# Kernel optimization log

Measured on AMD Instinct MI355X. Metric: run time of the kernel, lower is better.

Reference implementation:

```python
import jax, jax.numpy as jnp
import numpy as np

BN_EPS = 1e-5
LEAKY_SLOPE = 0.01

N_TOTAL, FEAT_DIM = 100000, 128
N_BATCH, K = 50000, 16
EMBED_DIM = 128


def setup_inputs() -> dict:
    key = jax.random.key(0)
    k1, k2, k3 = jax.random.split(key, 3)
    raw_features = jax.random.normal(k1, (N_TOTAL, FEAT_DIM), dtype=jnp.float32)
    weight = jax.random.normal(k2, (FEAT_DIM, EMBED_DIM), dtype=jnp.float32) * (1.0 / np.sqrt(FEAT_DIM))
    gamma = jnp.ones((EMBED_DIM,), dtype=jnp.float32)
    beta = jnp.zeros((EMBED_DIM,), dtype=jnp.float32)
    neigh_idx = jax.random.randint(k3, (N_BATCH, K), 0, N_TOTAL, dtype=jnp.int64)
    return {"raw_features": raw_features, "weight": weight, "gamma": gamma,
            "beta": beta, "neigh_idx": neigh_idx}


def reference(raw_features, weight, gamma, beta, neigh_idx):
    # Mean aggregation over sampled neighbors: [N_BATCH, K, F] -> [N_BATCH, F]
    neigh_feats = jnp.mean(raw_features[neigh_idx], axis=1)
    # Dense transform: [N_BATCH, EMBED_DIM]
    x = neigh_feats @ weight
    # BatchNorm1d (training mode: batch statistics, biased variance)
    mean = jnp.mean(x, axis=0)
    var = jnp.var(x, axis=0)
    x = (x - mean) * jax.lax.rsqrt(var + BN_EPS) * gamma + beta
    # LeakyReLU (default negative_slope=0.01)
    return jnp.where(x >= 0, x, LEAKY_SLOPE * x)
```

## Files before the change

kernel.cpp:

```cpp
#include <hip/hip_runtime.h>
#include <hip/hip_bf16.h>


#define NTOTAL 100000
#define FEAT   128
#define NB     50000
#define KNEI   16
#define NTILES (NB / 16)

#define OFF_STATS 0
#define OFF_WT    1024
#define OFF_RAWB  33792
#define OFF_XB    (33792 + 25600000)
#define WS_NEEDED (OFF_XB + 12800000)

typedef float f32x4 __attribute__((ext_vector_type(4)));
typedef short bf16x8 __attribute__((ext_vector_type(8)));

__device__ __forceinline__ unsigned short f2bf(float f) {
    union { float f; unsigned u; } v; v.f = f;
    unsigned r = v.u + 0x7FFF + ((v.u >> 16) & 1);
    return (unsigned short)(r >> 16);
}

#define WT_LD 136
#define A_LD  136

__global__ __launch_bounds__(256) void enc_conv(
    const float* __restrict__ raw, const float* __restrict__ W,
    unsigned short* __restrict__ rawb, unsigned short* __restrict__ Wt,
    float* __restrict__ gstats)
{
    const int t = threadIdx.x;
    if (blockIdx.x < 64) {
        int e = blockIdx.x * 256 + t;
        int n = e >> 7, k = e & 127;
        Wt[e] = f2bf(W[k * FEAT + n]);
    }
    if (blockIdx.x == 64 && t < 2 * FEAT) gstats[t] = 0.f;

    const float4* raw4 = (const float4*)raw;
    ushort4* rb4 = (ushort4*)rawb;
    const int NQ = NTOTAL * FEAT / 4;
    for (int e = blockIdx.x * 256 + t; e < NQ; e += gridDim.x * 256) {
        float4 v = raw4[e];
        ushort4 b;
        b.x = f2bf(v.x); b.y = f2bf(v.y); b.z = f2bf(v.z); b.w = f2bf(v.w);
        rb4[e] = b;
    }
}

__global__ __launch_bounds__(256, 4) void enc_gemm_b(
    const unsigned short* __restrict__ rawb, const unsigned short* __restrict__ Wt,
    const int* __restrict__ idx, unsigned short* __restrict__ xb,
    float* __restrict__ gstats)
{
    __shared__ unsigned short sWt[128 * WT_LD];
    __shared__ unsigned short sA[16 * A_LD];
    __shared__ int sidx[256];

    const int t = threadIdx.x;

    #pragma unroll
    for (int i = 0; i < 8; ++i) {
        int e = t + i * 256;
        int n = e >> 4, c = e & 15;
        *(uint4*)&sWt[n * WT_LD + c * 8] = *(const uint4*)&Wt[n * 128 + c * 8];
    }

    const int lane = t & 63;
    const int wv = t >> 6;
    const int ln = lane & 15;
    const int qd = lane >> 4;
    const int c2 = t & 15;
    const int g  = t >> 4;
    const int n0 = wv * 32 + ln, n1 = n0 + 16;

    float s1a = 0.f, s2a = 0.f, s1b = 0.f, s2b = 0.f;

    for (int tile = blockIdx.x; tile < NTILES; tile += gridDim.x) {
        const int i0 = tile * 16;
        __syncthreads();
        sidx[t] = idx[i0 * KNEI + t];
        __syncthreads();

        {
            const int* ip = &sidx[g * KNEI];
            uint4 v[16];
            #pragma unroll
            for (int k = 0; k < KNEI; ++k)
                v[k] = *(const uint4*)&rawb[(size_t)ip[k] * FEAT + c2 * 8];
            __builtin_amdgcn_sched_barrier(0);
            float a0=0.f,a1=0.f,a2=0.f,a3=0.f,a4=0.f,a5=0.f,a6=0.f,a7=0.f;
            #pragma unroll
            for (int k = 0; k < KNEI; ++k) {
                a0 += __uint_as_float(v[k].x << 16);
                a1 += __uint_as_float(v[k].x & 0xFFFF0000u);
                a2 += __uint_as_float(v[k].y << 16);
                a3 += __uint_as_float(v[k].y & 0xFFFF0000u);
                a4 += __uint_as_float(v[k].z << 16);
                a5 += __uint_as_float(v[k].z & 0xFFFF0000u);
                a6 += __uint_as_float(v[k].w << 16);
                a7 += __uint_as_float(v[k].w & 0xFFFF0000u);
            }
            uint4 b;
            b.x = (unsigned)f2bf(a0 * 0.0625f) | ((unsigned)f2bf(a1 * 0.0625f) << 16);
            b.y = (unsigned)f2bf(a2 * 0.0625f) | ((unsigned)f2bf(a3 * 0.0625f) << 16);
            b.z = (unsigned)f2bf(a4 * 0.0625f) | ((unsigned)f2bf(a5 * 0.0625f) << 16);
            b.w = (unsigned)f2bf(a6 * 0.0625f) | ((unsigned)f2bf(a7 * 0.0625f) << 16);
            *(uint4*)&sA[g * A_LD + c2 * 8] = b;
        }
        __syncthreads();

        f32x4 acc0 = {0.f, 0.f, 0.f, 0.f}, acc1 = {0.f, 0.f, 0.f, 0.f};
        #pragma unroll
        for (int kt = 0; kt < 4; ++kt) {
            const int k0 = kt * 32 + qd * 8;
            bf16x8 a  = *(const bf16x8*)&sA[ln * A_LD + k0];
            bf16x8 b0 = *(const bf16x8*)&sWt[n0 * WT_LD + k0];
            bf16x8 b1 = *(const bf16x8*)&sWt[n1 * WT_LD + k0];
            acc0 = __builtin_amdgcn_mfma_f32_16x16x32_bf16(a, b0, acc0, 0, 0, 0);
            acc1 = __builtin_amdgcn_mfma_f32_16x16x32_bf16(a, b1, acc1, 0, 0, 0);
        }

        #pragma unroll
        for (int ri = 0; ri < 4; ++ri) {
            const int row = i0 + qd * 4 + ri;
            float v0 = acc0[ri], v1 = acc1[ri];
            xb[row * FEAT + n0] = f2bf(v0);
            xb[row * FEAT + n1] = f2bf(v1);
            s1a += v0; s2a += v0 * v0;
            s1b += v1; s2b += v1 * v1;
        }
    }

    s1a += __shfl_down(s1a, 32); s1a += __shfl_down(s1a, 16);
    s2a += __shfl_down(s2a, 32); s2a += __shfl_down(s2a, 16);
    s1b += __shfl_down(s1b, 32); s1b += __shfl_down(s1b, 16);
    s2b += __shfl_down(s2b, 32); s2b += __shfl_down(s2b, 16);
    if (qd == 0) {
        atomicAdd(&gstats[n0], s1a);
        atomicAdd(&gstats[FEAT + n0], s2a);
        atomicAdd(&gstats[n1], s1b);
        atomicAdd(&gstats[FEAT + n1], s2b);
    }
}

__global__ __launch_bounds__(256) void enc_bn_b(
    const unsigned short* __restrict__ xb, float* __restrict__ out,
    const float* __restrict__ gstats,
    const float* __restrict__ gamma, const float* __restrict__ beta)
{
    __shared__ float sScale[FEAT], sShift[FEAT];
    const int t = threadIdx.x;
    if (t < FEAT) {
        float s1 = gstats[t], s2 = gstats[FEAT + t];
        float mean = s1 * (1.0f / NB);
        float var = s2 * (1.0f / NB) - mean * mean;
        float sc = gamma[t] * rsqrtf(var + 1e-5f);
        sScale[t] = sc;
        sShift[t] = beta[t] - mean * sc;
    }
    __syncthreads();

    const int f8 = (t & 15) * 8;
    const float4 sc0 = *(const float4*)&sScale[f8], sc1 = *(const float4*)&sScale[f8 + 4];
    const float4 sh0 = *(const float4*)&sShift[f8], sh1 = *(const float4*)&sShift[f8 + 4];

    const uint4* x4 = (const uint4*)xb;
    float4* o4 = (float4*)out;
    const int total8 = NB * FEAT / 8;
    for (int e = blockIdx.x * 256 + t; e < total8; e += gridDim.x * 256) {
        uint4 v = x4[e];
        float4 r0, r1; float y;
        y = __uint_as_float(v.x << 16)        * sc0.x + sh0.x; r0.x = (y >= 0.f) ? y : 0.01f * y;
        y = __uint_as_float(v.x & 0xFFFF0000u)* sc0.y + sh0.y; r0.y = (y >= 0.f) ? y : 0.01f * y;
        y = __uint_as_float(v.y << 16)        * sc0.z + sh0.z; r0.z = (y >= 0.f) ? y : 0.01f * y;
        y = __uint_as_float(v.y & 0xFFFF0000u)* sc0.w + sh0.w; r0.w = (y >= 0.f) ? y : 0.01f * y;
        y = __uint_as_float(v.z << 16)        * sc1.x + sh1.x; r1.x = (y >= 0.f) ? y : 0.01f * y;
        y = __uint_as_float(v.z & 0xFFFF0000u)* sc1.y + sh1.y; r1.y = (y >= 0.f) ? y : 0.01f * y;
        y = __uint_as_float(v.w << 16)        * sc1.z + sh1.z; r1.z = (y >= 0.f) ? y : 0.01f * y;
        y = __uint_as_float(v.w & 0xFFFF0000u)* sc1.w + sh1.w; r1.w = (y >= 0.f) ? y : 0.01f * y;
        o4[e * 2] = r0; o4[e * 2 + 1] = r1;
    }
}

__global__ __launch_bounds__(256, 4) void enc_gemm_f(
    const float* __restrict__ raw, const float* __restrict__ W,
    const int* __restrict__ idx, float* __restrict__ out,
    float* __restrict__ gstats)
{
    __shared__ unsigned short sWt[128 * WT_LD];
    __shared__ unsigned short sA[16 * A_LD];
    __shared__ int sidx[256];
    const int t = threadIdx.x;
    #pragma unroll 4
    for (int i = 0; i < 64; ++i) {
        int e = t + i * 256;
        int f = e >> 7, n = e & 127;
        sWt[n * WT_LD + f] = f2bf(W[e]);
    }
    const int lane = t & 63, wv = t >> 6, ln = lane & 15, qd = lane >> 4;
    const int c = t & 31, g = t >> 5;
    const int n0 = wv * 32 + ln, n1 = n0 + 16;
    float s1a = 0.f, s2a = 0.f, s1b = 0.f, s2b = 0.f;
    const float4* raw4 = (const float4*)raw;
    for (int tile = blockIdx.x; tile < NTILES; tile += gridDim.x) {
        const int i0 = tile * 16;
        __syncthreads();
        sidx[t] = idx[i0 * KNEI + t];
        __syncthreads();
        #pragma unroll
        for (int rr = 0; rr < 2; ++rr) {
            const int r = g * 2 + rr;
            const int* ip = &sidx[r * KNEI];
            float4 acc = {0.f, 0.f, 0.f, 0.f};
            #pragma unroll
            for (int k = 0; k < KNEI; ++k) {
                float4 v = raw4[(size_t)ip[k] * 32 + c];
                acc.x += v.x; acc.y += v.y; acc.z += v.z; acc.w += v.w;
            }
            ushort4 b;
            b.x = f2bf(acc.x * 0.0625f); b.y = f2bf(acc.y * 0.0625f);
            b.z = f2bf(acc.z * 0.0625f); b.w = f2bf(acc.w * 0.0625f);
            *(ushort4*)&sA[r * A_LD + c * 4] = b;
        }
        __syncthreads();
        f32x4 acc0 = {0.f, 0.f, 0.f, 0.f}, acc1 = {0.f, 0.f, 0.f, 0.f};
        #pragma unroll
        for (int kt = 0; kt < 4; ++kt) {
            const int k0 = kt * 32 + qd * 8;
            bf16x8 a  = *(const bf16x8*)&sA[ln * A_LD + k0];
            bf16x8 b0 = *(const bf16x8*)&sWt[n0 * WT_LD + k0];
            bf16x8 b1 = *(const bf16x8*)&sWt[n1 * WT_LD + k0];
            acc0 = __builtin_amdgcn_mfma_f32_16x16x32_bf16(a, b0, acc0, 0, 0, 0);
            acc1 = __builtin_amdgcn_mfma_f32_16x16x32_bf16(a, b1, acc1, 0, 0, 0);
        }
        #pragma unroll
        for (int ri = 0; ri < 4; ++ri) {
            const int row = i0 + qd * 4 + ri;
            float v0 = acc0[ri], v1 = acc1[ri];
            out[row * FEAT + n0] = v0;
            out[row * FEAT + n1] = v1;
            s1a += v0; s2a += v0 * v0;
            s1b += v1; s2b += v1 * v1;
        }
    }
    s1a += __shfl_down(s1a, 32); s1a += __shfl_down(s1a, 16);
    s2a += __shfl_down(s2a, 32); s2a += __shfl_down(s2a, 16);
    s1b += __shfl_down(s1b, 32); s1b += __shfl_down(s1b, 16);
    s2b += __shfl_down(s2b, 32); s2b += __shfl_down(s2b, 16);
    if (qd == 0) {
        atomicAdd(&gstats[n0], s1a);
        atomicAdd(&gstats[FEAT + n0], s2a);
        atomicAdd(&gstats[n1], s1b);
        atomicAdd(&gstats[FEAT + n1], s2b);
    }
}

__global__ __launch_bounds__(256) void enc_bn_f(
    float* __restrict__ out, const float* __restrict__ gstats,
    const float* __restrict__ gamma, const float* __restrict__ beta)
{
    __shared__ float sScale[FEAT], sShift[FEAT];
    const int t = threadIdx.x;
    if (t < FEAT) {
        float s1 = gstats[t], s2 = gstats[FEAT + t];
        float mean = s1 * (1.0f / NB);
        float var = s2 * (1.0f / NB) - mean * mean;
        float sc = gamma[t] * rsqrtf(var + 1e-5f);
        sScale[t] = sc;
        sShift[t] = beta[t] - mean * sc;
    }
    __syncthreads();
    const int f4 = (t & 31) * 4;
    const float4 sc = *(const float4*)&sScale[f4];
    const float4 sh = *(const float4*)&sShift[f4];
    const int total4 = NB * FEAT / 4;
    float4* o4 = (float4*)out;
    for (int e = blockIdx.x * 256 + t; e < total4; e += gridDim.x * 256) {
        float4 v = o4[e];
        float4 r; float y;
        y = v.x * sc.x + sh.x; r.x = (y >= 0.f) ? y : 0.01f * y;
        y = v.y * sc.y + sh.y; r.y = (y >= 0.f) ? y : 0.01f * y;
        y = v.z * sc.z + sh.z; r.z = (y >= 0.f) ? y : 0.01f * y;
        y = v.w * sc.w + sh.w; r.w = (y >= 0.f) ? y : 0.01f * y;
        o4[e] = r;
    }
}

extern "C" void kernel_launch(void* const* d_in, const int* in_sizes, int n_in,
                              void* d_out, int out_size, void* d_ws, size_t ws_size,
                              hipStream_t stream) {
    const float* raw   = (const float*)d_in[0];
    const float* W     = (const float*)d_in[1];
    const float* gamma = (const float*)d_in[2];
    const float* beta  = (const float*)d_in[3];
    const int*   idx   = (const int*)d_in[4];
    float* out = (float*)d_out;

    char* ws = (char*)d_ws;
    float* gstats = (float*)(ws + OFF_STATS);

    if (ws_size >= WS_NEEDED) {
        unsigned short* Wt   = (unsigned short*)(ws + OFF_WT);
        unsigned short* rawb = (unsigned short*)(ws + OFF_RAWB);
        unsigned short* xb   = (unsigned short*)(ws + OFF_XB);
        enc_conv<<<2048, 256, 0, stream>>>(raw, W, rawb, Wt, gstats);
        enc_gemm_b<<<1024, 256, 0, stream>>>(rawb, Wt, idx, xb, gstats);
        enc_bn_b<<<1024, 256, 0, stream>>>(xb, out, gstats, gamma, beta);
    } else {
        hipMemsetAsync(gstats, 0, 2 * FEAT * sizeof(float), stream);
        enc_gemm_f<<<1024, 256, 0, stream>>>(raw, W, idx, out, gstats);
        enc_bn_f<<<1024, 256, 0, stream>>>(out, gstats, gamma, beta);
    }
}
```

Measured before the change: 146.0 us.

## Transform all features by W first, then gather-mean the projected rows

Uses linearity of mean and matmul to apply the weight to all 100k raw rows first, producing a bf16 Z table. A separate gather kernel then averages 16 Z rows per output and computes the batch statistics. The separate conversion pass and the per-call W transpose buffer are removed, and W is converted inside the GEMM blocks. Statistics go through 8 slotted atomic partial buffers to cut contention. The trade-offs are that the GEMM now covers 100k rows instead of 50k, and rounding of the bf16 Z values happens before the mean.

```diff
diff --git a/kernel.cpp b/kernel.cpp
--- a/kernel.cpp
+++ b/kernel.cpp
@@ -7,11 +7,12 @@
 #define NB     50000
 #define KNEI   16
 #define NTILES (NB / 16)
-
-#define OFF_STATS 0
-#define OFF_WT    1024
-#define OFF_RAWB  33792
-#define OFF_XB    (33792 + 25600000)
+#define ZTILES (NTOTAL / 16)
+#define NSLOT  8
+
+#define OFF_PSTAT 0
+#define OFF_ZB    8192
+#define OFF_XB    (8192 + 25600000)
 #define WS_NEEDED (OFF_XB + 12800000)
 
 typedef float f32x4 __attribute__((ext_vector_type(4)));
@@ -26,46 +27,30 @@
 #define WT_LD 136
 #define A_LD  136
 
-__global__ __launch_bounds__(256) void enc_conv(
+__global__ __launch_bounds__(256, 4) void enc_zgemm(
     const float* __restrict__ raw, const float* __restrict__ W,
-    unsigned short* __restrict__ rawb, unsigned short* __restrict__ Wt,
-    float* __restrict__ gstats)
-{
-    const int t = threadIdx.x;
-    if (blockIdx.x < 64) {
-        int e = blockIdx.x * 256 + t;
-        int n = e >> 7, k = e & 127;
-        Wt[e] = f2bf(W[k * FEAT + n]);
-    }
-    if (blockIdx.x == 64 && t < 2 * FEAT) gstats[t] = 0.f;
-
-    const float4* raw4 = (const float4*)raw;
-    ushort4* rb4 = (ushort4*)rawb;
-    const int NQ = NTOTAL * FEAT / 4;
-    for (int e = blockIdx.x * 256 + t; e < NQ; e += gridDim.x * 256) {
-        float4 v = raw4[e];
-        ushort4 b;
-        b.x = f2bf(v.x); b.y = f2bf(v.y); b.z = f2bf(v.z); b.w = f2bf(v.w);
-        rb4[e] = b;
-    }
-}
-
-__global__ __launch_bounds__(256, 4) void enc_gemm_b(
-    const unsigned short* __restrict__ rawb, const unsigned short* __restrict__ Wt,
-    const int* __restrict__ idx, unsigned short* __restrict__ xb,
-    float* __restrict__ gstats)
+    unsigned short* __restrict__ Zb, float* __restrict__ pstats)
 {
     __shared__ unsigned short sWt[128 * WT_LD];
     __shared__ unsigned short sA[16 * A_LD];
-    __shared__ int sidx[256];
-
-    const int t = threadIdx.x;
-
-    #pragma unroll
-    for (int i = 0; i < 8; ++i) {
+
+    const int t = threadIdx.x;
+
+    if (blockIdx.x == 0) {
+        #pragma unroll
+        for (int i = 0; i < NSLOT; ++i) pstats[t + i * 256] = 0.f;
+    }
+
+    #pragma unroll
+    for (int i = 0; i < 16; ++i) {
         int e = t + i * 256;
-        int n = e >> 4, c = e & 15;
-        *(uint4*)&sWt[n * WT_LD + c * 8] = *(const uint4*)&Wt[n * 128 + c * 8];
+        float4 w4 = ((const float4*)W)[e];
+        int li = e * 4;
+        int k = li >> 7, n = li & 127;
+        sWt[(n + 0) * WT_LD + k] = f2bf(w4.x);
+        sWt[(n + 1) * WT_LD + k] = f2bf(w4.y);
+        sWt[(n + 2) * WT_LD + k] = f2bf(w4.z);
+        sWt[(n + 3) * WT_LD + k] = f2bf(w4.w);
     }
 
     const int lane = t & 63;
@@ -76,38 +61,17 @@
     const int g  = t >> 4;
     const int n0 = wv * 32 + ln, n1 = n0 + 16;
 
-    float s1a = 0.f, s2a = 0.f, s1b = 0.f, s2b = 0.f;
-
-    for (int tile = blockIdx.x; tile < NTILES; tile += gridDim.x) {
-        const int i0 = tile * 16;
-        __syncthreads();
-        sidx[t] = idx[i0 * KNEI + t];
-        __syncthreads();
-
+    for (int tile = blockIdx.x; tile < ZTILES; tile += gridDim.x) {
+        const int r0 = tile * 16;
+        __syncthreads();
         {
-            const int* ip = &sidx[g * KNEI];
-            uint4 v[16];
-            #pragma unroll
-            for (int k = 0; k < KNEI; ++k)
-                v[k] = *(const uint4*)&rawb[(size_t)ip[k] * FEAT + c2 * 8];
-            __builtin_amdgcn_sched_barrier(0);
-            float a0=0.f,a1=0.f,a2=0.f,a3=0.f,a4=0.f,a5=0.f,a6=0.f,a7=0.f;
-            #pragma unroll
-            for (int k = 0; k < KNEI; ++k) {
-                a0 += __uint_as_float(v[k].x << 16);
-                a1 += __uint_as_float(v[k].x & 0xFFFF0000u);
-                a2 += __uint_as_float(v[k].y << 16);
-                a3 += __uint_as_float(v[k].y & 0xFFFF0000u);
-                a4 += __uint_as_float(v[k].z << 16);
-                a5 += __uint_as_float(v[k].z & 0xFFFF0000u);
-                a6 += __uint_as_float(v[k].w << 16);
-                a7 += __uint_as_float(v[k].w & 0xFFFF0000u);
-            }
+            const float4* rp = (const float4*)&raw[(size_t)(r0 + g) * FEAT + c2 * 8];
+            float4 x0 = rp[0], x1 = rp[1];
             uint4 b;
-            b.x = (unsigned)f2bf(a0 * 0.0625f) | ((unsigned)f2bf(a1 * 0.0625f) << 16);
-            b.y = (unsigned)f2bf(a2 * 0.0625f) | ((unsigned)f2bf(a3 * 0.0625f) << 16);
-            b.z = (unsigned)f2bf(a4 * 0.0625f) | ((unsigned)f2bf(a5 * 0.0625f) << 16);
-            b.w = (unsigned)f2bf(a6 * 0.0625f) | ((unsigned)f2bf(a7 * 0.0625f) << 16);
+            b.x = (unsigned)f2bf(x0.x) | ((unsigned)f2bf(x0.y) << 16);
+            b.y = (unsigned)f2bf(x0.z) | ((unsigned)f2bf(x0.w) << 16);
+            b.z = (unsigned)f2bf(x1.x) | ((unsigned)f2bf(x1.y) << 16);
+            b.w = (unsigned)f2bf(x1.z) | ((unsigned)f2bf(x1.w) << 16);
             *(uint4*)&sA[g * A_LD + c2 * 8] = b;
         }
         __syncthreads();
@@ -125,36 +89,97 @@
 
         #pragma unroll
         for (int ri = 0; ri < 4; ++ri) {
-            const int row = i0 + qd * 4 + ri;
-            float v0 = acc0[ri], v1 = acc1[ri];
-            xb[row * FEAT + n0] = f2bf(v0);
-            xb[row * FEAT + n1] = f2bf(v1);
-            s1a += v0; s2a += v0 * v0;
-            s1b += v1; s2b += v1 * v1;
-        }
-    }
-
-    s1a += __shfl_down(s1a, 32); s1a += __shfl_down(s1a, 16);
-    s2a += __shfl_down(s2a, 32); s2a += __shfl_down(s2a, 16);
-    s1b += __shfl_down(s1b, 32); s1b += __shfl_down(s1b, 16);
-    s2b += __shfl_down(s2b, 32); s2b += __shfl_down(s2b, 16);
-    if (qd == 0) {
-        atomicAdd(&gstats[n0], s1a);
-        atomicAdd(&gstats[FEAT + n0], s2a);
-        atomicAdd(&gstats[n1], s1b);
-        atomicAdd(&gstats[FEAT + n1], s2b);
-    }
-}
-
-__global__ __launch_bounds__(256) void enc_bn_b(
+            const int row = r0 + qd * 4 + ri;
+            Zb[row * FEAT + n0] = f2bf(acc0[ri]);
+            Zb[row * FEAT + n1] = f2bf(acc1[ri]);
+        }
+    }
+}
+
+__global__ __launch_bounds__(256, 4) void enc_gather(
+    const unsigned short* __restrict__ Zb, const int* __restrict__ idx,
+    unsigned short* __restrict__ xb, float* __restrict__ pstats)
+{
+    __shared__ int sidx[256];
+    __shared__ float sRed[4 * 256];
+
+    const int t = threadIdx.x;
+    const int i0 = blockIdx.x * 16;
+
+    sidx[t] = idx[i0 * KNEI + t];
+    __syncthreads();
+
+    const int g = t >> 4, c2 = t & 15;
+    const int* ip = &sidx[g * KNEI];
+
+    uint4 v[16];
+    #pragma unroll
+    for (int k = 0; k < KNEI; ++k)
+        v[k] = *(const uint4*)&Zb[(size_t)ip[k] * FEAT + c2 * 8];
+    __builtin_amdgcn_sched_group_barrier(0x20, 16, 0);
+    __builtin_amdgcn_sched_barrier(0);
+
+    float a[8];
+    #pragma unroll
+    for (int j = 0; j < 8; ++j) a[j] = 0.f;
+    #pragma unroll
+    for (int k = 0; k < KNEI; ++k) {
+        a[0] += __uint_as_float(v[k].x << 16);
+        a[1] += __uint_as_float(v[k].x & 0xFFFF0000u);
+        a[2] += __uint_as_float(v[k].y << 16);
+        a[3] += __uint_as_float(v[k].y & 0xFFFF0000u);
+        a[4] += __uint_as_float(v[k].z << 16);
+        a[5] += __uint_as_float(v[k].z & 0xFFFF0000u);
+        a[6] += __uint_as_float(v[k].w << 16);
+        a[7] += __uint_as_float(v[k].w & 0xFFFF0000u);
+    }
+    #pragma unroll
+    for (int j = 0; j < 8; ++j) a[j] *= 0.0625f;
+
+    {
+        uint4 b;
+        b.x = (unsigned)f2bf(a[0]) | ((unsigned)f2bf(a[1]) << 16);
+        b.y = (unsigned)f2bf(a[2]) | ((unsigned)f2bf(a[3]) << 16);
+        b.z = (unsigned)f2bf(a[4]) | ((unsigned)f2bf(a[5]) << 16);
+        b.w = (unsigned)f2bf(a[6]) | ((unsigned)f2bf(a[7]) << 16);
+        *(uint4*)&xb[(size_t)(i0 + g) * FEAT + c2 * 8] = b;
+    }
+
+    float q[8];
+    #pragma unroll
+    for (int j = 0; j < 8; ++j) q[j] = a[j] * a[j];
+    #pragma unroll
+    for (int j = 0; j < 8; ++j) {
+        a[j] += __shfl_down(a[j], 32); a[j] += __shfl_down(a[j], 16);
+        q[j] += __shfl_down(q[j], 32); q[j] += __shfl_down(q[j], 16);
+    }
+    const int lane = t & 63, wv = t >> 6;
+    if (lane < 16) {
+        #pragma unroll
+        for (int j = 0; j < 8; ++j) {
+            sRed[wv * 256 + c2 * 8 + j]       = a[j];
+            sRed[wv * 256 + 128 + c2 * 8 + j] = q[j];
+        }
+    }
+    __syncthreads();
+    float s = sRed[t] + sRed[256 + t] + sRed[512 + t] + sRed[768 + t];
+    atomicAdd(&pstats[(blockIdx.x & (NSLOT - 1)) * 256 + t], s);
+}
+
+__global__ __launch_bounds__(256) void enc_bn(
     const unsigned short* __restrict__ xb, float* __restrict__ out,
-    const float* __restrict__ gstats,
+    const float* __restrict__ pstats,
     const float* __restrict__ gamma, const float* __restrict__ beta)
 {
     __shared__ float sScale[FEAT], sShift[FEAT];
     const int t = threadIdx.x;
     if (t < FEAT) {
-        float s1 = gstats[t], s2 = gstats[FEAT + t];
+        float s1 = 0.f, s2 = 0.f;
+        #pragma unroll
+        for (int sl = 0; sl < NSLOT; ++sl) {
+            s1 += pstats[sl * 256 + t];
+            s2 += pstats[sl * 256 + 128 + t];
+        }
         float mean = s1 * (1.0f / NB);
         float var = s2 * (1.0f / NB) - mean * mean;
         float sc = gamma[t] * rsqrtf(var + 1e-5f);
@@ -300,16 +325,16 @@
     float* out = (float*)d_out;
 
     char* ws = (char*)d_ws;
-    float* gstats = (float*)(ws + OFF_STATS);
 
     if (ws_size >= WS_NEEDED) {
-        unsigned short* Wt   = (unsigned short*)(ws + OFF_WT);
-        unsigned short* rawb = (unsigned short*)(ws + OFF_RAWB);
+        float* pstats        = (float*)(ws + OFF_PSTAT);
+        unsigned short* Zb   = (unsigned short*)(ws + OFF_ZB);
         unsigned short* xb   = (unsigned short*)(ws + OFF_XB);
-        enc_conv<<<2048, 256, 0, stream>>>(raw, W, rawb, Wt, gstats);
-        enc_gemm_b<<<1024, 256, 0, stream>>>(rawb, Wt, idx, xb, gstats);
-        enc_bn_b<<<1024, 256, 0, stream>>>(xb, out, gstats, gamma, beta);
+        enc_zgemm<<<1042, 256, 0, stream>>>(raw, W, Zb, pstats);
+        enc_gather<<<NTILES, 256, 0, stream>>>(Zb, idx, xb, pstats);
+        enc_bn<<<1024, 256, 0, stream>>>(xb, out, pstats, gamma, beta);
     } else {
+        float* gstats = (float*)(ws + OFF_PSTAT);
         hipMemsetAsync(gstats, 0, 2 * FEAT * sizeof(float), stream);
         enc_gemm_f<<<1024, 256, 0, stream>>>(raw, W, idx, out, gstats);
         enc_bn_f<<<1024, 256, 0, stream>>>(out, gstats, gamma, beta);
```

Measured after the change: 152.3 us. +4.3%, slower.
